# Kernel tuning notes

Hardware: AMD Instinct MI355X
Metric: run time of the kernel (lower is better)

The kernel has to match this reference:

```python
import jax, jax.numpy as jnp
import numpy as np

B, N, E = 8, 4096, 524288
BN = B * N


def setup_inputs() -> dict:
    key = jax.random.key(0)
    ks = jax.random.split(key, 24)
    def w(k, shape):
        return jax.random.normal(k, shape, dtype=jnp.float32) * 0.05
    return {
        "x": jax.random.normal(ks[0], (B, 3, N), dtype=jnp.float32),
        "emb": jax.random.normal(ks[1], (B, 32, N), dtype=jnp.float32),
        "edge_index": jax.random.randint(ks[2], (2, E), 0, BN),
        "e": 0,
        "g_w": w(ks[3], (3, 64)),   "g_b": jnp.zeros((64,), jnp.float32),
        "c_w": w(ks[4], (32, 64)),  "c_b": jnp.zeros((64,), jnp.float32),
        "m1_w1": w(ks[5], (64, 128)),  "m1_b1": jnp.zeros((128,), jnp.float32),
        "m1_w2": w(ks[6], (128, 128)), "m1_b2": jnp.zeros((128,), jnp.float32),
        "m2_w1": w(ks[7], (128, 128)), "m2_b1": jnp.zeros((128,), jnp.float32),
        "m2_w2": w(ks[8], (128, 256)), "m2_b2": jnp.zeros((256,), jnp.float32),
        "m3_w1": w(ks[9], (512, 512)), "m3_b1": jnp.zeros((512,), jnp.float32),
        "m3_w2": w(ks[10], (512, 1024)), "m3_b2": jnp.zeros((1024,), jnp.float32),
        "fc_w": w(ks[11], (64, 256)), "fc_b": jnp.zeros((256,), jnp.float32),
    }


def reference(x, emb, edge_index, e,
              g_w, g_b, c_w, c_b,
              m1_w1, m1_b1, m1_w2, m1_b2,
              m2_w1, m2_b1, m2_w2, m2_b2,
              m3_w1, m3_b1, m3_w2, m3_b2,
              fc_w, fc_b):
    # Conv1d with kernel_size=1 == per-point linear: [B,Cin,N] -> [B,Cout,N]
    xg = jax.nn.relu(jnp.einsum('bcn,cd->bdn', x, g_w) + g_b[None, :, None])
    ce = jax.nn.relu(jnp.einsum('bcn,cd->bdn', emb, c_w) + c_b[None, :, None])
    feat = ce if e == 1 else xg                       # [B,64,N]
    f = feat.transpose(0, 2, 1).reshape(-1, 64)        # [B*N,64]

    src, tgt = edge_index[0], edge_index[1]

    def gin(h, w1, b1, w2, b2):
        # GINConv (eps=0): mlp(h + sum_{j->i} h_j)
        agg = jax.ops.segment_sum(h[src], tgt, num_segments=BN)
        z = h + agg
        return jax.nn.relu(z @ w1 + b1) @ w2 + b2

    f1 = jax.nn.relu(gin(f, m1_w1, m1_b1, m1_w2, m1_b2))    # [B*N,128]
    f2 = jax.nn.relu(gin(f1, m2_w1, m2_b1, m2_w2, m2_b2))   # [B*N,256]
    feat1 = f1.reshape(B, N, 128).transpose(0, 2, 1)        # [B,128,N]
    feat2 = f2.reshape(B, N, 256).transpose(0, 2, 1)        # [B,256,N]

    oth_in = xg if e == 1 else ce                           # other modality
    oth = jax.nn.relu(jnp.einsum('bcn,cd->bnd', oth_in, fc_w) + fc_b)  # [B,N,256]
    oth = oth.transpose(0, 2, 1)                            # [B,256,N]

    fused = jnp.concatenate([feat2, oth], axis=1)           # [B,512,N]
    ff = fused.transpose(0, 2, 1).reshape(-1, 512)          # [B*N,512]
    f3 = gin(ff, m3_w1, m3_b1, m3_w2, m3_b2)                # [B*N,1024]
    feat3 = f3.reshape(B, N, 1024).transpose(0, 2, 1)       # [B,1024,N]

    return jnp.concatenate([feat1, feat2, feat3], axis=1)   # [B,1408,N]
```

## Files before the change

### kernel.cpp

```cpp
#include <hip/hip_runtime.h>

#define BN_   32768
#define NN    4096
#define EDGES 524288
#define DEGCAP 64

typedef __attribute__((ext_vector_type(8))) __bf16 bf16x8;
typedef __attribute__((ext_vector_type(4))) float f32x4;

__global__ void build_adj(const int* __restrict__ src, const int* __restrict__ tgt,
                          int* __restrict__ cnt, int* __restrict__ adj){
  int i = blockIdx.x*256 + threadIdx.x;
  if (i < EDGES){
    int t = tgt[i];
    int pos = atomicAdd(&cnt[t], 1);
    if (pos < DEGCAP) adj[(size_t)t*DEGCAP + pos] = src[i];
  }
}

__global__ void wtrans_all(const float* __restrict__ w11, const float* __restrict__ w12,
                           const float* __restrict__ w21, const float* __restrict__ w22,
                           const float* __restrict__ w31, const float* __restrict__ w32,
                           __bf16* o11, __bf16* o12, __bf16* o21, __bf16* o22,
                           __bf16* o31, __bf16* o32)
{
  int idx = blockIdx.x*256 + threadIdx.x;
  const float* src; __bf16* d; int N, K, base;
  if (idx < 8192)        { src=w11; d=o11; K=64;  N=128;  base=0; }
  else if (idx < 24576)  { src=w12; d=o12; K=128; N=128;  base=8192; }
  else if (idx < 40960)  { src=w21; d=o21; K=128; N=128;  base=24576; }
  else if (idx < 73728)  { src=w22; d=o22; K=128; N=256;  base=40960; }
  else if (idx < 335872) { src=w31; d=o31; K=512; N=512;  base=73728; }
  else if (idx < 860160) { src=w32; d=o32; K=512; N=1024; base=335872; }
  else return;
  int t = idx - base;
  int k = t / N, n = t - k*N;
  d[(size_t)n*K + k] = (__bf16)src[t];
}

__global__ __launch_bounds__(256)
void conv_kernel(const float* __restrict__ x, const float* __restrict__ emb,
                 const int* __restrict__ eflag,
                 const float* __restrict__ g_w, const float* __restrict__ g_b,
                 const float* __restrict__ c_w, const float* __restrict__ c_b,
                 const float* __restrict__ fc_w, const float* __restrict__ fc_b,
                 __bf16* __restrict__ F0, __bf16* __restrict__ FF)
{
  __shared__ float xs[3][16];
  __shared__ float es[32][16];
  __shared__ float sel[16][64];
  const int tid = threadIdx.x;
  const int node0 = blockIdx.x * 16;
  const int b  = node0 >> 12;
  const int nl = node0 & 4095;
  const int e  = *eflag;

  if (tid < 48){
    int c = tid >> 4, i = tid & 15;
    xs[c][i] = x[(size_t)b*3*NN + c*NN + nl + i];
  }
  {
    int idx = tid;
#pragma unroll
    for (int p=0;p<2;p++){
      int c = idx >> 4, i = idx & 15;
      es[c][i] = emb[(size_t)b*32*NN + c*NN + nl + i];
      idx += 256;
    }
  }
  __syncthreads();
  {
    const int ch = tid & 63;
    const int g  = tid >> 6;
    float gw[3], cw[32];
#pragma unroll
    for (int c=0;c<3;c++)  gw[c] = g_w[c*64 + ch];
#pragma unroll
    for (int c=0;c<32;c++) cw[c] = c_w[c*64 + ch];
    float gb = g_b[ch], cb = c_b[ch];
#pragma unroll
    for (int q=0;q<4;q++){
      int n = g*4 + q;
      float a = gb;
#pragma unroll
      for (int c=0;c<3;c++) a += xs[c][n]*gw[c];
      float xg = fmaxf(a, 0.f);
      float s2 = cb;
#pragma unroll
      for (int c=0;c<32;c++) s2 += es[c][n]*cw[c];
      float ce = fmaxf(s2, 0.f);
      float f0 = e ? ce : xg;
      float so = e ? xg : ce;
      F0[(size_t)(node0+n)*64 + ch] = (__bf16)f0;
      sel[n][ch] = so;
    }
  }
  __syncthreads();
  {
    const int h = tid;
    float acc[16];
#pragma unroll
    for (int i=0;i<16;i++) acc[i]=0.f;
    for (int k4=0;k4<16;k4++){
      float w0 = fc_w[(k4*4+0)*256 + h];
      float w1 = fc_w[(k4*4+1)*256 + h];
      float w2 = fc_w[(k4*4+2)*256 + h];
      float w3 = fc_w[(k4*4+3)*256 + h];
#pragma unroll
      for (int i=0;i<16;i++){
        float4 sv = *(const float4*)&sel[i][k4*4];
        acc[i] += sv.x*w0 + sv.y*w1 + sv.z*w2 + sv.w*w3;
      }
    }
    float fb = fc_b[h];
#pragma unroll
    for (int i=0;i<16;i++){
      float v = fmaxf(acc[i] + fb, 0.f);
      FF[(size_t)(node0+i)*512 + 256 + h] = (__bf16)v;
    }
  }
}

template<int C>
__global__ __launch_bounds__(256)
void gather_k(const __bf16* __restrict__ f, const int* __restrict__ cnt,
              const int* __restrict__ adj, __bf16* __restrict__ z)
{
  constexpr int TPN = C/8;
  const int tid  = threadIdx.x;
  int node = blockIdx.x*(256/TPN) + tid/TPN;
  if (TPN == 64) node = __builtin_amdgcn_readfirstlane(node);
  const int c8   = (tid & (TPN-1))*8;
  const int deg  = min(cnt[node], DEGCAP);
  const int* __restrict__ arow = adj + (size_t)node*DEGCAP;
  const __bf16* p = f + c8;
  float a[8];
  {
    bf16x8 sv = *(const bf16x8*)(p + (size_t)node*C);
#pragma unroll
    for (int t=0;t<8;t++) a[t] = (float)sv[t];
  }
  int j = 0;
  for (; j+8<=deg; j+=8){
    int sIdx[8];
#pragma unroll
    for (int u=0;u<8;u++) sIdx[u] = arow[j+u];
    bf16x8 v[8];
#pragma unroll
    for (int u=0;u<8;u++) v[u] = *(const bf16x8*)(p + (size_t)sIdx[u]*C);
#pragma unroll
    for (int u=0;u<8;u++)
#pragma unroll
      for (int t=0;t<8;t++) a[t] += (float)v[u][t];
  }
  for (; j+2<=deg; j+=2){
    int s0=arow[j], s1=arow[j+1];
    bf16x8 v0=*(const bf16x8*)(p+(size_t)s0*C), v1=*(const bf16x8*)(p+(size_t)s1*C);
#pragma unroll
    for (int t=0;t<8;t++) a[t] += (float)v0[t] + (float)v1[t];
  }
  if (j < deg){
    int s=arow[j];
    bf16x8 v=*(const bf16x8*)(p+(size_t)s*C);
#pragma unroll
    for (int t=0;t<8;t++) a[t] += (float)v[t];
  }
  bf16x8 o;
#pragma unroll
  for (int t=0;t<8;t++) o[t] = (__bf16)a[t];
  *(bf16x8*)(z + (size_t)node*C + c8) = o;
}

template<int K, int GSWAP>
__global__ __launch_bounds__(256, 2)
void mfma_gemm(const __bf16* __restrict__ A, const __bf16* __restrict__ B,
               const float* __restrict__ bias,
               __bf16* __restrict__ outr, int ostride,
               float* __restrict__ outT, int cbase, int relu)
{
  constexpr int NK = K/32;
  __shared__ __align__(16) char smem[32768];

  const int tid = threadIdx.x;
  const int l   = tid & 63;
  const int w   = tid >> 6;
  const int wm  = w >> 1, wn = w & 1;
  const int n0  = (GSWAP ? blockIdx.y : blockIdx.x) * 128;
  const int h0  = (GSWAP ? blockIdx.x : blockIdx.y) * 128;

  f32x4 acc[4][4];
#pragma unroll
  for (int m=0;m<4;m++)
#pragma unroll
    for (int n=0;n<4;n++) acc[m][n] = (f32x4){0.f,0.f,0.f,0.f};

  const __bf16* gsrc = (w<2) ? A : B;
  const int soff = (w<2) ? 0 : 8192;
  const int rbase = (w<2) ? n0 : h0;
  const int ci0 = (w & 1) * 4;
  const int cd = (l&3) ^ ((l>>3)&3);
  const __bf16* g0 = gsrc + (size_t)(rbase + (l>>2))*K + cd*8;

  const int r16 = l & 15, q = l >> 4;
  const int fsw = ((q ^ ((r16>>1)&3)) << 4);

  auto STAGE = [&](int ks, int bb){
    char* d = smem + bb*16384 + soff;
    const __bf16* gk = g0 + ks*32;
#pragma unroll
    for (int i=0;i<4;i++){
      __builtin_amdgcn_global_load_lds(
        (const __attribute__((address_space(1))) void*)(gk + (size_t)(ci0+i)*16*K),
        (__attribute__((address_space(3))) void*)(d + (ci0+i)*1024), 16, 0, 0);
    }
  };

  STAGE(0, 0);
  STAGE(1, 1);

  for (int ks=0; ks<NK; ks++){
    const int bb = ks & 1;
    if (ks < NK-1) asm volatile("s_waitcnt vmcnt(4)" ::: "memory");
    else           asm volatile("s_waitcnt vmcnt(0)" ::: "memory");
    asm volatile("s_barrier" ::: "memory");

    const char* base = smem + bb*16384;
    bf16x8 fa[4], fb[4];
#pragma unroll
    for (int m=0;m<4;m++){
      const int ro = (wm*64 + m*16 + r16)*64 + fsw;
      fa[m] = *(const bf16x8*)(base + ro);
    }
#pragma unroll
    for (int n=0;n<4;n++){
      const int ro = (wn*64 + n*16 + r16)*64 + fsw;
      fb[n] = *(const bf16x8*)(base + 8192 + ro);
    }
    asm volatile("s_waitcnt lgkmcnt(0)" ::: "memory");
    __builtin_amdgcn_sched_barrier(0);

    __builtin_amdgcn_s_setprio(1);
#pragma unroll
    for (int m=0;m<4;m++)
#pragma unroll
      for (int n=0;n<4;n++)
        acc[m][n] = __builtin_amdgcn_mfma_f32_16x16x32_bf16(fa[m], fb[n], acc[m][n], 0,0,0);
    __builtin_amdgcn_s_setprio(0);

    asm volatile("s_barrier" ::: "memory");
    if (ks+2 < NK) STAGE(ks+2, bb);
  }

  __syncthreads();
  float* scratch = (float*)(void*)smem + w*1088;

  float bv[4];
#pragma unroll
  for (int n=0;n<4;n++) bv[n] = bias[h0 + wn*64 + n*16 + r16];

#pragma unroll
  for (int m=0;m<4;m++){
#pragma unroll
    for (int n=0;n<4;n++)
#pragma unroll
      for (int r=0;r<4;r++){
        float v = acc[m][n][r] + bv[n];
        if (relu) v = fmaxf(v, 0.f);
        scratch[(q*4+r)*68 + n*16 + r16] = v;
      }
    if (outr){
      const int row = l>>2, ch = (l&3)*16;
      bf16x8 H0,H1;
#pragma unroll
      for (int t=0;t<16;t++){
        float x = scratch[row*68 + ch + t];
        if (t<8) H0[t]=(__bf16)x; else H1[t-8]=(__bf16)x;
      }
      size_t o = (size_t)(n0 + wm*64 + m*16 + row)*ostride + h0 + wn*64 + ch;
      *(bf16x8*)(outr+o)   = H0;
      *(bf16x8*)(outr+o+8) = H1;
    }
    if (outT){
      const int b = n0 >> 12, nl = n0 & 4095;
      const int rr0 = (l&3)*4;
#pragma unroll
      for (int j=0;j<4;j++){
        const int c = (l>>2) + 16*j;
        f32x4 v;
#pragma unroll
        for (int i=0;i<4;i++) v[i] = scratch[(rr0+i)*68 + c];
        size_t o = ((size_t)b*1408 + cbase + h0 + wn*64 + c)*NN + nl + wm*64 + m*16 + rr0;
        *(f32x4*)(outT + o) = v;
      }
    }
  }
}

extern "C" void kernel_launch(void* const* d_in, const int* in_sizes, int n_in,
                              void* d_out, int out_size, void* d_ws, size_t ws_size,
                              hipStream_t stream)
{
  const float* x     = (const float*)d_in[0];
  const float* emb   = (const float*)d_in[1];
  const int*   ei    = (const int*)d_in[2];
  const int*   eflag = (const int*)d_in[3];
  const float* g_w   = (const float*)d_in[4];
  const float* g_b   = (const float*)d_in[5];
  const float* c_w   = (const float*)d_in[6];
  const float* c_b   = (const float*)d_in[7];
  const float* m1w1  = (const float*)d_in[8];
  const float* m1b1  = (const float*)d_in[9];
  const float* m1w2  = (const float*)d_in[10];
  const float* m1b2  = (const float*)d_in[11];
  const float* m2w1  = (const float*)d_in[12];
  const float* m2b1  = (const float*)d_in[13];
  const float* m2w2  = (const float*)d_in[14];
  const float* m2b2  = (const float*)d_in[15];
  const float* m3w1  = (const float*)d_in[16];
  const float* m3b1  = (const float*)d_in[17];
  const float* m3w2  = (const float*)d_in[18];
  const float* m3b2  = (const float*)d_in[19];
  const float* fc_w  = (const float*)d_in[20];
  const float* fc_b  = (const float*)d_in[21];
  float* out = (float*)d_out;
  char*  ws  = (char*)d_ws;

  __bf16* F0 = (__bf16*)(ws + 0);
  __bf16* Z1 = (__bf16*)(ws + 4194304);
  __bf16* H1 = (__bf16*)(ws + 8388608);
  __bf16* F1 = (__bf16*)(ws + 16777216);
  __bf16* Z2 = (__bf16*)(ws + 25165824);
  __bf16* H2 = (__bf16*)(ws + 33554432);
  __bf16* FF = (__bf16*)(ws + 41943040);
  __bf16* Z3 = (__bf16*)(ws + 75497472);
  __bf16* H3 = (__bf16*)(ws + 109051904);
  char* wb = ws + 150994944;
  __bf16* W11=(__bf16*)(wb+0);
  __bf16* W12=(__bf16*)(wb+16384);
  __bf16* W21=(__bf16*)(wb+49152);
  __bf16* W22=(__bf16*)(wb+81920);
  __bf16* W31=(__bf16*)(wb+147456);
  __bf16* W32=(__bf16*)(wb+671744);
  int* adj = (int*)(ws + 153092096);
  int* cnt = (int*)(ws + 161480704);

  const int* srcp = ei;
  const int* tgtp = ei + EDGES;

  hipMemsetAsync(cnt, 0, BN_*4, stream);
  build_adj<<<EDGES/256, 256, 0, stream>>>(srcp, tgtp, cnt, adj);

  conv_kernel<<<BN_/16, 256, 0, stream>>>(x, emb, eflag, g_w, g_b, c_w, c_b,
                                          fc_w, fc_b, F0, FF);

  wtrans_all<<<3360, 256, 0, stream>>>(m1w1, m1w2, m2w1, m2w2, m3w1, m3w2,
                                       W11, W12, W21, W22, W31, W32);

  gather_k<64><<<BN_/32, 256, 0, stream>>>(F0, cnt, adj, Z1);
  mfma_gemm<64,0><<<dim3(BN_/128, 1), 256, 0, stream>>>(
      Z1, W11, m1b1, H1, 128, nullptr, 0, 1);
  mfma_gemm<128,0><<<dim3(BN_/128, 1), 256, 0, stream>>>(
      H1, W12, m1b2, F1, 128, out, 0, 1);

  gather_k<128><<<BN_/16, 256, 0, stream>>>(F1, cnt, adj, Z2);
  mfma_gemm<128,0><<<dim3(BN_/128, 1), 256, 0, stream>>>(
      Z2, W21, m2b1, H2, 128, nullptr, 0, 1);
  mfma_gemm<128,0><<<dim3(BN_/128, 2), 256, 0, stream>>>(
      H2, W22, m2b2, FF, 512, out, 128, 1);

  gather_k<512><<<BN_/4, 256, 0, stream>>>(FF, cnt, adj, Z3);
  mfma_gemm<512,1><<<dim3(4, BN_/128), 256, 0, stream>>>(
      Z3, W31, m3b1, H3, 512, nullptr, 0, 1);
  mfma_gemm<512,1><<<dim3(8, BN_/128), 256, 0, stream>>>(
      H3, W32, m3b2, nullptr, 0, out, 384, 0);
}
```

Before: 311.2 us.

## Merge prep kernels into one launch and use 256-row tiles for big GEMMs

Three preprocessing kernels (adjacency build, pointwise convs, weight transpose/cast) are combined into one launch, with the work chosen by block index, which removes launch gaps. The two large layer-3 GEMMs move to a new 512-thread kernel with 256x128 tiles, where the B tile is shared across twice as many rows. This cuts redundant weight loads per output. It raises LDS use to 48KB and register pressure, which may reduce occupancy.

```diff
diff --git a/kernel.cpp b/kernel.cpp
--- a/kernel.cpp
+++ b/kernel.cpp
@@ -8,49 +8,52 @@
 typedef __attribute__((ext_vector_type(8))) __bf16 bf16x8;
 typedef __attribute__((ext_vector_type(4))) float f32x4;
 
-__global__ void build_adj(const int* __restrict__ src, const int* __restrict__ tgt,
-                          int* __restrict__ cnt, int* __restrict__ adj){
-  int i = blockIdx.x*256 + threadIdx.x;
-  if (i < EDGES){
-    int t = tgt[i];
-    int pos = atomicAdd(&cnt[t], 1);
-    if (pos < DEGCAP) adj[(size_t)t*DEGCAP + pos] = src[i];
-  }
-}
-
-__global__ void wtrans_all(const float* __restrict__ w11, const float* __restrict__ w12,
-                           const float* __restrict__ w21, const float* __restrict__ w22,
-                           const float* __restrict__ w31, const float* __restrict__ w32,
-                           __bf16* o11, __bf16* o12, __bf16* o21, __bf16* o22,
-                           __bf16* o31, __bf16* o32)
-{
-  int idx = blockIdx.x*256 + threadIdx.x;
-  const float* src; __bf16* d; int N, K, base;
-  if (idx < 8192)        { src=w11; d=o11; K=64;  N=128;  base=0; }
-  else if (idx < 24576)  { src=w12; d=o12; K=128; N=128;  base=8192; }
-  else if (idx < 40960)  { src=w21; d=o21; K=128; N=128;  base=24576; }
-  else if (idx < 73728)  { src=w22; d=o22; K=128; N=256;  base=40960; }
-  else if (idx < 335872) { src=w31; d=o31; K=512; N=512;  base=73728; }
-  else if (idx < 860160) { src=w32; d=o32; K=512; N=1024; base=335872; }
-  else return;
-  int t = idx - base;
-  int k = t / N, n = t - k*N;
-  d[(size_t)n*K + k] = (__bf16)src[t];
-}
-
 __global__ __launch_bounds__(256)
-void conv_kernel(const float* __restrict__ x, const float* __restrict__ emb,
+void prep_kernel(const int* __restrict__ src, const int* __restrict__ tgt,
+                 int* __restrict__ cnt, int* __restrict__ adj,
+                 const float* __restrict__ x, const float* __restrict__ emb,
                  const int* __restrict__ eflag,
                  const float* __restrict__ g_w, const float* __restrict__ g_b,
                  const float* __restrict__ c_w, const float* __restrict__ c_b,
                  const float* __restrict__ fc_w, const float* __restrict__ fc_b,
-                 __bf16* __restrict__ F0, __bf16* __restrict__ FF)
+                 __bf16* __restrict__ F0, __bf16* __restrict__ FF,
+                 const float* __restrict__ w11, const float* __restrict__ w12,
+                 const float* __restrict__ w21, const float* __restrict__ w22,
+                 const float* __restrict__ w31, const float* __restrict__ w32,
+                 __bf16* __restrict__ o11, __bf16* __restrict__ o12,
+                 __bf16* __restrict__ o21, __bf16* __restrict__ o22,
+                 __bf16* __restrict__ o31, __bf16* __restrict__ o32)
 {
+  const int bx = blockIdx.x;
+  const int tid = threadIdx.x;
+
+  if (bx < 2048){
+    int i = bx*256 + tid;
+    int t = tgt[i];
+    int pos = atomicAdd(&cnt[t], 1);
+    if (pos < DEGCAP) adj[(size_t)t*DEGCAP + pos] = src[i];
+    return;
+  }
+  if (bx >= 4096){
+    int idx = (bx - 4096)*256 + tid;
+    const float* s; __bf16* d; int N, K, base;
+    if (idx < 8192)        { s=w11; d=o11; K=64;  N=128;  base=0; }
+    else if (idx < 24576)  { s=w12; d=o12; K=128; N=128;  base=8192; }
+    else if (idx < 40960)  { s=w21; d=o21; K=128; N=128;  base=24576; }
+    else if (idx < 73728)  { s=w22; d=o22; K=128; N=256;  base=40960; }
+    else if (idx < 335872) { s=w31; d=o31; K=512; N=512;  base=73728; }
+    else if (idx < 860160) { s=w32; d=o32; K=512; N=1024; base=335872; }
+    else return;
+    int t = idx - base;
+    int k = t / N, n = t - k*N;
+    d[(size_t)n*K + k] = (__bf16)s[t];
+    return;
+  }
+
   __shared__ float xs[3][16];
   __shared__ float es[32][16];
   __shared__ float sel[16][64];
-  const int tid = threadIdx.x;
-  const int node0 = blockIdx.x * 16;
+  const int node0 = (bx - 2048) * 16;
   const int b  = node0 >> 12;
   const int nl = node0 & 4095;
   const int e  = *eflag;
@@ -227,15 +230,11 @@
     const char* base = smem + bb*16384;
     bf16x8 fa[4], fb[4];
 #pragma unroll
-    for (int m=0;m<4;m++){
-      const int ro = (wm*64 + m*16 + r16)*64 + fsw;
-      fa[m] = *(const bf16x8*)(base + ro);
-    }
-#pragma unroll
-    for (int n=0;n<4;n++){
-      const int ro = (wn*64 + n*16 + r16)*64 + fsw;
-      fb[n] = *(const bf16x8*)(base + 8192 + ro);
-    }
+    for (int m=0;m<4;m++)
+      fa[m] = *(const bf16x8*)(base + (wm*64 + m*16 + r16)*64 + fsw);
+#pragma unroll
+    for (int n=0;n<4;n++)
+      fb[n] = *(const bf16x8*)(base + 8192 + (wn*64 + n*16 + r16)*64 + fsw);
     asm volatile("s_waitcnt lgkmcnt(0)" ::: "memory");
     __builtin_amdgcn_sched_barrier(0);
 
@@ -273,8 +272,142 @@
       bf16x8 H0,H1;
 #pragma unroll
       for (int t=0;t<16;t++){
-        float x = scratch[row*68 + ch + t];
-        if (t<8) H0[t]=(__bf16)x; else H1[t-8]=(__bf16)x;
+        float xv = scratch[row*68 + ch + t];
+        if (t<8) H0[t]=(__bf16)xv; else H1[t-8]=(__bf16)xv;
+      }
+      size_t o = (size_t)(n0 + wm*64 + m*16 + row)*ostride + h0 + wn*64 + ch;
+      *(bf16x8*)(outr+o)   = H0;
+      *(bf16x8*)(outr+o+8) = H1;
+    }
+    if (outT){
+      const int b = n0 >> 12, nl = n0 & 4095;
+      const int rr0 = (l&3)*4;
+#pragma unroll
+      for (int j=0;j<4;j++){
+        const int c = (l>>2) + 16*j;
+        f32x4 v;
+#pragma unroll
+        for (int i=0;i<4;i++) v[i] = scratch[(rr0+i)*68 + c];
+        size_t o = ((size_t)b*1408 + cbase + h0 + wn*64 + c)*NN + nl + wm*64 + m*16 + rr0;
+        *(f32x4*)(outT + o) = v;
+      }
+    }
+  }
+}
+
+template<int K, int GSWAP>
+__global__ __launch_bounds__(512, 2)
+void mfma_gemm256(const __bf16* __restrict__ A, const __bf16* __restrict__ B,
+                  const float* __restrict__ bias,
+                  __bf16* __restrict__ outr, int ostride,
+                  float* __restrict__ outT, int cbase, int relu)
+{
+  constexpr int NK = K/32;
+  __shared__ __align__(16) char smem[49152];
+
+  const int tid = threadIdx.x;
+  const int l   = tid & 63;
+  const int w   = tid >> 6;
+  const int wm  = w >> 1, wn = w & 1;
+  const int n0  = (GSWAP ? blockIdx.y : blockIdx.x) * 256;
+  const int h0  = (GSWAP ? blockIdx.x : blockIdx.y) * 128;
+
+  f32x4 acc[4][4];
+#pragma unroll
+  for (int m=0;m<4;m++)
+#pragma unroll
+    for (int n=0;n<4;n++) acc[m][n] = (f32x4){0.f,0.f,0.f,0.f};
+
+  const bool isA = (w < 4);
+  const __bf16* gsrc = isA ? A : B;
+  const int rbase = isA ? (n0 + w*64) : (h0 + (w-4)*32);
+  const int soff  = isA ? (w*4096) : (16384 + (w-4)*2048);
+  const int cd = (l&3) ^ ((l>>3)&3);
+  const __bf16* g0 = gsrc + (size_t)(rbase + (l>>2))*K + cd*8;
+
+  const int r16 = l & 15, q = l >> 4;
+  const int fsw = ((q ^ ((r16>>1)&3)) << 4);
+
+  auto STAGE = [&](int ks, int bb){
+    char* d = smem + bb*24576 + soff;
+    const __bf16* gk = g0 + ks*32;
+    if (isA){
+#pragma unroll
+      for (int i=0;i<4;i++){
+        __builtin_amdgcn_global_load_lds(
+          (const __attribute__((address_space(1))) void*)(gk + (size_t)i*16*K),
+          (__attribute__((address_space(3))) void*)(d + i*1024), 16, 0, 0);
+      }
+    } else {
+#pragma unroll
+      for (int i=0;i<2;i++){
+        __builtin_amdgcn_global_load_lds(
+          (const __attribute__((address_space(1))) void*)(gk + (size_t)i*16*K),
+          (__attribute__((address_space(3))) void*)(d + i*1024), 16, 0, 0);
+      }
+    }
+  };
+
+  STAGE(0, 0);
+  STAGE(1, 1);
+
+  for (int ks=0; ks<NK; ks++){
+    const int bb = ks & 1;
+    if (ks < NK-1){
+      if (isA) asm volatile("s_waitcnt vmcnt(4)" ::: "memory");
+      else     asm volatile("s_waitcnt vmcnt(2)" ::: "memory");
+    } else {
+      asm volatile("s_waitcnt vmcnt(0)" ::: "memory");
+    }
+    asm volatile("s_barrier" ::: "memory");
+
+    const char* base = smem + bb*24576;
+    bf16x8 fa[4], fb[4];
+#pragma unroll
+    for (int m=0;m<4;m++)
+      fa[m] = *(const bf16x8*)(base + (wm*64 + m*16 + r16)*64 + fsw);
+#pragma unroll
+    for (int n=0;n<4;n++)
+      fb[n] = *(const bf16x8*)(base + 16384 + (wn*64 + n*16 + r16)*64 + fsw);
+    asm volatile("s_waitcnt lgkmcnt(0)" ::: "memory");
+    __builtin_amdgcn_sched_barrier(0);
+
+    __builtin_amdgcn_s_setprio(1);
+#pragma unroll
+    for (int m=0;m<4;m++)
+#pragma unroll
+      for (int n=0;n<4;n++)
+        acc[m][n] = __builtin_amdgcn_mfma_f32_16x16x32_bf16(fa[m], fb[n], acc[m][n], 0,0,0);
+    __builtin_amdgcn_s_setprio(0);
+
+    asm volatile("s_barrier" ::: "memory");
+    if (ks+2 < NK) STAGE(ks+2, bb);
+  }
+
+  __syncthreads();
+  float* scratch = (float*)(void*)smem + w*1088;
+
+  float bv[4];
+#pragma unroll
+  for (int n=0;n<4;n++) bv[n] = bias[h0 + wn*64 + n*16 + r16];
+
+#pragma unroll
+  for (int m=0;m<4;m++){
+#pragma unroll
+    for (int n=0;n<4;n++)
+#pragma unroll
+      for (int r=0;r<4;r++){
+        float v = acc[m][n][r] + bv[n];
+        if (relu) v = fmaxf(v, 0.f);
+        scratch[(q*4+r)*68 + n*16 + r16] = v;
+      }
+    if (outr){
+      const int row = l>>2, ch = (l&3)*16;
+      bf16x8 H0,H1;
+#pragma unroll
+      for (int t=0;t<16;t++){
+        float xv = scratch[row*68 + ch + t];
+        if (t<8) H0[t]=(__bf16)xv; else H1[t-8]=(__bf16)xv;
       }
       size_t o = (size_t)(n0 + wm*64 + m*16 + row)*ostride + h0 + wn*64 + ch;
       *(bf16x8*)(outr+o)   = H0;
@@ -348,13 +481,9 @@
   const int* tgtp = ei + EDGES;
 
   hipMemsetAsync(cnt, 0, BN_*4, stream);
-  build_adj<<<EDGES/256, 256, 0, stream>>>(srcp, tgtp, cnt, adj);
-
-  conv_kernel<<<BN_/16, 256, 0, stream>>>(x, emb, eflag, g_w, g_b, c_w, c_b,
-                                          fc_w, fc_b, F0, FF);
-
-  wtrans_all<<<3360, 256, 0, stream>>>(m1w1, m1w2, m2w1, m2w2, m3w1, m3w2,
-                                       W11, W12, W21, W22, W31, W32);
+  prep_kernel<<<7456, 256, 0, stream>>>(srcp, tgtp, cnt, adj,
+      x, emb, eflag, g_w, g_b, c_w, c_b, fc_w, fc_b, F0, FF,
+      m1w1, m1w2, m2w1, m2w2, m3w1, m3w2, W11, W12, W21, W22, W31, W32);
 
   gather_k<64><<<BN_/32, 256, 0, stream>>>(F0, cnt, adj, Z1);
   mfma_gemm<64,0><<<dim3(BN_/128, 1), 256, 0, stream>>>(
@@ -369,8 +498,8 @@
       H2, W22, m2b2, FF, 512, out, 128, 1);
 
   gather_k<512><<<BN_/4, 256, 0, stream>>>(FF, cnt, adj, Z3);
-  mfma_gemm<512,1><<<dim3(4, BN_/128), 256, 0, stream>>>(
+  mfma_gemm256<512,1><<<dim3(4, BN_/256), 512, 0, stream>>>(
       Z3, W31, m3b1, H3, 512, nullptr, 0, 1);
-  mfma_gemm<512,1><<<dim3(8, BN_/128), 256, 0, stream>>>(
+  mfma_gemm256<512,1><<<dim3(8, BN_/256), 512, 0, stream>>>(
       H3, W32, m3b2, nullptr, 0, out, 384, 0);
 }
```

After: 326.4 us. +4.9%, slower.
